# Performance work log

Measured on AMD Instinct MI355X. Metric: run time of the kernel, lower is better.

Reference implementation:

```python
import jax, jax.numpy as jnp
import numpy as np

N, E, B = 50000, 400000, 16
H, D = 4, 64  # heads, per-head out feats
NUM_LAYERS = 4
NEG_SLOPE = 0.2


def setup_inputs() -> dict:
    key = jax.random.key(0)
    ks = jax.random.split(key, 12)
    inp = {
        "feat": jax.random.normal(ks[0], (N, 16), jnp.float32),
        "is_root": jax.random.uniform(ks[1], (N,), jnp.float32),
        "src": jax.random.randint(ks[2], (E,), 0, N, jnp.int32),
        "dst": jax.random.randint(ks[3], (E,), 0, N, jnp.int32),
        "graph_id": jnp.sort(jax.random.randint(ks[4], (N,), 0, B, jnp.int32)),
        "W_in": jax.random.normal(ks[5], (16, 64), jnp.float32) / jnp.sqrt(16.0),
        "b_in": jnp.zeros((64,), jnp.float32),
        "W_src": jax.random.normal(ks[6], (128, 256), jnp.float32) / jnp.sqrt(128.0),
        "b_src": jnp.zeros((256,), jnp.float32),
        "W_dst": jax.random.normal(ks[7], (128, 256), jnp.float32) / jnp.sqrt(128.0),
        "b_dst": jnp.zeros((256,), jnp.float32),
        "attn": jax.random.normal(ks[8], (H, D), jnp.float32) / jnp.sqrt(float(D)),
        "W_out": jax.random.normal(ks[9], (64, 32), jnp.float32) / jnp.sqrt(64.0),
        "b_out": jnp.zeros((32,), jnp.float32),
    }
    return inp


def _gatv2_layer(x, W_src, b_src, W_dst, b_dst, attn, src, dst, n_nodes):
    # DGL GATv2Conv: e_ij = a . LeakyReLU(W_src x_j + W_dst x_i); softmax over in-edges of i.
    fs = (x @ W_src + b_src).reshape(n_nodes, H, D)
    fd = (x @ W_dst + b_dst).reshape(n_nodes, H, D)
    e = jax.nn.leaky_relu(fs[src] + fd[dst], NEG_SLOPE)          # [E,H,D]
    logits = jnp.einsum("ehd,hd->eh", e, attn)                    # [E,H]
    m = jax.ops.segment_max(logits, dst, num_segments=n_nodes)    # [N,H]
    ex = jnp.exp(logits - m[dst])
    denom = jax.ops.segment_sum(ex, dst, num_segments=n_nodes)    # [N,H]
    alpha = ex / denom[dst]                                       # [E,H]
    msg = fs[src] * alpha[:, :, None]                             # [E,H,D]
    rst = jax.ops.segment_sum(msg, dst, num_segments=n_nodes)     # [N,H,D]
    return jnp.tanh(rst)


def reference(feat, is_root, src, dst, graph_id,
              W_in, b_in, W_src, b_src, W_dst, b_dst, attn, W_out, b_out):
    n_nodes = feat.shape[0]
    h0 = feat @ W_in + b_in                                       # [N,64]
    h = h0
    for _ in range(NUM_LAYERS):
        x = jnp.concatenate([h, h0], axis=1)                      # [N,128]
        h = _gatv2_layer(x, W_src, b_src, W_dst, b_dst, attn, src, dst, n_nodes).sum(axis=1)  # [N,64]
    hg = jax.ops.segment_sum(h * is_root[:, None], graph_id, num_segments=B)  # [B,64]
    return hg @ W_out + b_out                                     # [B,32]
```

## Files before the change

### kernel.cpp

```cpp
#include <hip/hip_runtime.h>
#include <math.h>

#define N_NODES 50000
#define N_EDGES 400000
#define N_GRAPHS 16
#define HEADS 4
#define NEG_SLOPE 0.2f
#define MAX_DEG 64

typedef __attribute__((ext_vector_type(8))) short short8;
typedef __attribute__((ext_vector_type(4))) float floatx4;
typedef _Float16 half_t;
typedef _Float16 half2_t __attribute__((ext_vector_type(2)));
typedef _Float16 half4_t __attribute__((ext_vector_type(4)));

__device__ __forceinline__ unsigned short f2bf(float x) {
    union { float f; unsigned int u; } v; v.f = x;
    unsigned int r = v.u + 0x7fffu + ((v.u >> 16) & 1u);
    return (unsigned short)(r >> 16);
}
__device__ __forceinline__ float bf2f(unsigned short b) {
    union { unsigned int u; float f; } v; v.u = ((unsigned int)b) << 16;
    return v.f;
}
__device__ __forceinline__ half2_t u2h2(unsigned int u) {
    union { unsigned int i; half2_t h; } v; v.i = u;
    return v.h;
}
__device__ __forceinline__ float fast_tanh(float x) {
    float e = __expf(2.f * x);
    return 1.f - 2.f / (e + 1.f);
}
__device__ __forceinline__ half2_t lrelu2(half2_t e) {
    half2_t s = e * (half2_t){(half_t)NEG_SLOPE, (half_t)NEG_SLOPE};
    return __builtin_elementwise_max(e, s);
}
__device__ __forceinline__ float dot2acc(half2_t a, half2_t b, float c) {
#if __has_builtin(__builtin_amdgcn_fdot2)
    return __builtin_amdgcn_fdot2(a, b, c, false);
#else
    return c + (float)a[0] * (float)b[0] + (float)a[1] * (float)b[1];
#endif
}

__global__ __launch_bounds__(256) void k_h0_pack(const float* __restrict__ feat,
                                                 const float* __restrict__ W_in,
                                                 const float* __restrict__ b_in,
                                                 unsigned short* __restrict__ h0,
                                                 const float* __restrict__ Wsrc,
                                                 const float* __restrict__ Wdst,
                                                 unsigned short* __restrict__ Wpack,
                                                 int* __restrict__ cursor,
                                                 float* __restrict__ hg) {
    int bid = blockIdx.x;
    if (bid < 12500) {
        int idx = bid * 256 + threadIdx.x;
        int node = idx >> 6, d = idx & 63;
        float acc = b_in[d];
        #pragma unroll
        for (int k = 0; k < 16; k++) acc += feat[node * 16 + k] * W_in[k * 64 + d];
        h0[idx] = f2bf(acc);
    } else if (bid < 12756) {
        int pb = bid - 12500;
        int mat = pb >> 7;
        int idx = (pb & 127) * 256 + threadIdx.x;
        const float* W = mat ? Wdst : Wsrc;
        int j = idx & 7;
        int lane = (idx >> 3) & 63;
        int q = (idx >> 9) & 3;
        int t = (idx >> 11) & 15;
        int col = t * 16 + (lane & 15);
        int k = q * 32 + (lane >> 4) * 8 + j;
        Wpack[mat * 32768 + idx] = f2bf(W[k * 256 + col]);
    } else if (bid < 12952) {
        int idx = (bid - 12756) * 256 + threadIdx.x;
        if (idx < N_NODES) cursor[idx] = 0;
    } else {
        for (int i = threadIdx.x; i < N_GRAPHS * 64; i += 256) hg[i] = 0.f;
    }
}

__global__ __launch_bounds__(256) void k_fill(const int* __restrict__ src, const int* __restrict__ dst,
                                              int* __restrict__ cursor, int* __restrict__ csr_pad, int e) {
    int i = blockIdx.x * 256 + threadIdx.x;
    if (i >= e) return;
    int d = dst[i];
    int slot = atomicAdd(&cursor[d], 1);
    if (slot < MAX_DEG) csr_pad[d * MAX_DEG + slot] = src[i];
}

__global__ __launch_bounds__(256) void k_gemm(const unsigned short* __restrict__ h,
                                              const unsigned short* __restrict__ h0,
                                              const unsigned short* __restrict__ Wpack,
                                              const float* __restrict__ bsrc,
                                              const float* __restrict__ bdst,
                                              half_t* __restrict__ fs,
                                              half_t* __restrict__ fd, int n) {
    __shared__ half_t tile[32][264];
    int mat = blockIdx.y;
    const unsigned short* Wp = Wpack + mat * 32768;
    const float* bias = mat ? bdst : bsrc;
    half_t* out = mat ? fd : fs;
    int wave = threadIdx.x >> 6, lane = threadIdx.x & 63;
    int quad = lane >> 4, m16 = lane & 15;
    int fhalf = wave & 1;
    int ngrp = wave >> 1;
    int node0 = blockIdx.x * 32 + ngrp * 16;

    floatx4 acc[8];
    #pragma unroll
    for (int t = 0; t < 8; t++) acc[t] = (floatx4){0.f, 0.f, 0.f, 0.f};

    int r = node0 + m16;
    if (r > n - 1) r = n - 1;

    #pragma unroll
    for (int q = 0; q < 4; q++) {
        int kk = q * 32 + quad * 8;
        const unsigned short* base = (kk < 64) ? (h + (size_t)r * 64 + kk)
                                               : (h0 + (size_t)r * 64 + (kk - 64));
        short8 x = *(const short8*)base;
        #pragma unroll
        for (int t = 0; t < 8; t++) {
            int tt = fhalf * 8 + t;
            short8 w = *(const short8*)(Wp + ((size_t)(tt * 4 + q) * 64 + lane) * 8);
            acc[t] = __builtin_amdgcn_mfma_f32_16x16x32_bf16(w, x, acc[t], 0, 0, 0);
        }
    }
    int lrow = ngrp * 16 + m16;
    #pragma unroll
    for (int t = 0; t < 8; t++) {
        int fbase = (fhalf * 8 + t) * 16 + quad * 4;
        float4 bb = *(const float4*)(bias + fbase);
        half4_t ov = { (half_t)(acc[t][0] + bb.x), (half_t)(acc[t][1] + bb.y),
                       (half_t)(acc[t][2] + bb.z), (half_t)(acc[t][3] + bb.w) };
        *(half4_t*)&tile[lrow][fbase] = ov;
    }
    __syncthreads();
    int base = blockIdx.x * 32;
    for (int i = threadIdx.x; i < 1024; i += 256) {
        int row = i >> 5, seg = i & 31;
        int node = base + row;
        if (node < n) {
            uint4 v = *(const uint4*)&tile[row][seg * 8];
            *(uint4*)(out + (size_t)node * 256 + seg * 8) = v;
        }
    }
}

__global__ __launch_bounds__(256) void k_agg(const half_t* __restrict__ fs,
                                             const half_t* __restrict__ fd,
                                             const int* __restrict__ cnt,
                                             const int* __restrict__ csr_pad,
                                             const float* __restrict__ attn,
                                             unsigned short* __restrict__ hout, int n) {
    int wave = threadIdx.x >> 6;
    int lane = threadIdx.x & 63;
    int node = blockIdx.x * 4 + wave;
    if (node >= n) return;
    int slot = lane >> 5;
    int foff = ((lane >> 3) & 3) * 64 + (lane & 7) * 8;
    unsigned boff = (unsigned)foff * 2;
    const char* fsb = (const char*)fs;

    int eraw = csr_pad[node * MAX_DEG + lane];
    int deg  = cnt[node];
    uint4 ufd = *(const uint4*)(fd + (size_t)node * 256 + foff);

    half2_t at2[4];
    {
        float4 a0 = *(const float4*)(attn + foff);
        float4 a1 = *(const float4*)(attn + foff + 4);
        at2[0] = (half2_t){(half_t)a0.x, (half_t)a0.y};
        at2[1] = (half2_t){(half_t)a0.z, (half_t)a0.w};
        at2[2] = (half2_t){(half_t)a1.x, (half_t)a1.y};
        at2[3] = (half2_t){(half_t)a1.z, (half_t)a1.w};
    }
    half2_t fd2[4] = {u2h2(ufd.x), u2h2(ufd.y), u2h2(ufd.z), u2h2(ufd.w)};

    if (deg > MAX_DEG) deg = MAX_DEG;
    int eid = (lane < deg) ? eraw : 0;

    float l = 0.f;
    half2_t zero2 = {(half_t)0.f, (half_t)0.f};
    half2_t acc2[4] = {zero2, zero2, zero2, zero2};

    int j = 0;
    do {
        int i0 = j + slot, i1 = j + 2 + slot, i2 = j + 4 + slot, i3 = j + 6 + slot;
        bool v0 = i0 < deg, v1 = i1 < deg, v2 = i2 < deg, v3 = i3 < deg;
        int s0 = __shfl(eid, i0 & 63, 64);
        int s1 = __shfl(eid, i1 & 63, 64);
        int s2 = __shfl(eid, i2 & 63, 64);
        int s3 = __shfl(eid, i3 & 63, 64);
        uint4 g0 = *(const uint4*)(fsb + (((unsigned)s0 << 9) + boff));
        uint4 g1 = *(const uint4*)(fsb + (((unsigned)s1 << 9) + boff));
        uint4 g2 = *(const uint4*)(fsb + (((unsigned)s2 << 9) + boff));
        uint4 g3 = *(const uint4*)(fsb + (((unsigned)s3 << 9) + boff));
        half2_t f0[4] = {u2h2(g0.x), u2h2(g0.y), u2h2(g0.z), u2h2(g0.w)};
        half2_t f1[4] = {u2h2(g1.x), u2h2(g1.y), u2h2(g1.z), u2h2(g1.w)};
        half2_t f2[4] = {u2h2(g2.x), u2h2(g2.y), u2h2(g2.z), u2h2(g2.w)};
        half2_t f3[4] = {u2h2(g3.x), u2h2(g3.y), u2h2(g3.z), u2h2(g3.w)};
        float p0 = 0.f, p1 = 0.f, p2 = 0.f, p3 = 0.f;
        #pragma unroll
        for (int k = 0; k < 4; k++) {
            p0 = dot2acc(at2[k], lrelu2(f0[k] + fd2[k]), p0);
            p1 = dot2acc(at2[k], lrelu2(f1[k] + fd2[k]), p1);
            p2 = dot2acc(at2[k], lrelu2(f2[k] + fd2[k]), p2);
            p3 = dot2acc(at2[k], lrelu2(f3[k] + fd2[k]), p3);
        }
        p0 += __shfl_xor(p0, 1, 64); p1 += __shfl_xor(p1, 1, 64);
        p2 += __shfl_xor(p2, 1, 64); p3 += __shfl_xor(p3, 1, 64);
        p0 += __shfl_xor(p0, 2, 64); p1 += __shfl_xor(p1, 2, 64);
        p2 += __shfl_xor(p2, 2, 64); p3 += __shfl_xor(p3, 2, 64);
        p0 += __shfl_xor(p0, 4, 64); p1 += __shfl_xor(p1, 4, 64);
        p2 += __shfl_xor(p2, 4, 64); p3 += __shfl_xor(p3, 4, 64);
        float w0 = v0 ? __expf(fminf(p0, 80.f)) : 0.f;
        float w1 = v1 ? __expf(fminf(p1, 80.f)) : 0.f;
        float w2 = v2 ? __expf(fminf(p2, 80.f)) : 0.f;
        float w3 = v3 ? __expf(fminf(p3, 80.f)) : 0.f;
        l += (w0 + w1) + (w2 + w3);
        half_t hw0 = (half_t)w0, hw1 = (half_t)w1, hw2 = (half_t)w2, hw3 = (half_t)w3;
        half2_t w02 = {hw0, hw0}, w12 = {hw1, hw1}, w22 = {hw2, hw2}, w32 = {hw3, hw3};
        #pragma unroll
        for (int k = 0; k < 4; k++) {
            acc2[k] += w02 * f0[k];
            acc2[k] += w12 * f1[k];
            acc2[k] += w22 * f2[k];
            acc2[k] += w32 * f3[k];
        }
        j += 8;
    } while (j < deg);
    l += __shfl_xor(l, 32, 64);
    #pragma unroll
    for (int k = 0; k < 4; k++) {
        float t = __builtin_bit_cast(float, acc2[k]);
        t = __shfl_xor(t, 32, 64);
        acc2[k] += __builtin_bit_cast(half2_t, t);
    }

    float inv = (l > 0.f) ? 1.f / l : 0.f;
    half2_t a0 = slot ? acc2[2] : acc2[0];
    half2_t a1 = slot ? acc2[3] : acc2[1];
    float o0 = fast_tanh((float)a0[0] * inv);
    float o1 = fast_tanh((float)a0[1] * inv);
    float o2 = fast_tanh((float)a1[0] * inv);
    float o3 = fast_tanh((float)a1[1] * inv);
    o0 += __shfl_xor(o0, 8, 64);  o0 += __shfl_xor(o0, 16, 64);
    o1 += __shfl_xor(o1, 8, 64);  o1 += __shfl_xor(o1, 16, 64);
    o2 += __shfl_xor(o2, 8, 64);  o2 += __shfl_xor(o2, 16, 64);
    o3 += __shfl_xor(o3, 8, 64);  o3 += __shfl_xor(o3, 16, 64);
    if ((lane & 31) < 8) {
        ushort4 ov = {f2bf(o0), f2bf(o1), f2bf(o2), f2bf(o3)};
        *(ushort4*)(hout + (size_t)node * 64 + (lane & 7) * 8 + slot * 4) = ov;
    }
}

__global__ __launch_bounds__(256) void k_readout(const unsigned short* __restrict__ h,
                                                 const float* __restrict__ is_root,
                                                 const int* __restrict__ gid, float* __restrict__ hg, int n) {
    int wave = threadIdx.x >> 6, lane = threadIdx.x & 63;
    int start = blockIdx.x * 128 + wave * 32;
    if (start >= n) return;
    int stop = min(start + 32, n);
    float acc = 0.f;
    int cur = gid[start];
    for (int i = start; i < stop; i++) {
        int g = gid[i];
        if (g != cur) {
            atomicAdd(&hg[cur * 64 + lane], acc);
            acc = 0.f;
            cur = g;
        }
        acc += bf2f(h[(size_t)i * 64 + lane]) * is_root[i];
    }
    atomicAdd(&hg[cur * 64 + lane], acc);
}

__global__ __launch_bounds__(512) void k_out(const float* __restrict__ hg, const float* __restrict__ W_out,
                                             const float* __restrict__ b_out, float* __restrict__ out) {
    int t = threadIdx.x;
    if (t >= N_GRAPHS * 32) return;
    int b = t >> 5, c = t & 31;
    float a = b_out[c];
    #pragma unroll
    for (int d = 0; d < 64; d++) a += hg[b * 64 + d] * W_out[d * 32 + c];
    out[t] = a;
}

extern "C" void kernel_launch(void* const* d_in, const int* in_sizes, int n_in,
                              void* d_out, int out_size, void* d_ws, size_t ws_size,
                              hipStream_t stream) {
    const float* feat    = (const float*)d_in[0];
    const float* is_root = (const float*)d_in[1];
    const int*   src     = (const int*)d_in[2];
    const int*   dst     = (const int*)d_in[3];
    const int*   gid     = (const int*)d_in[4];
    const float* W_in    = (const float*)d_in[5];
    const float* b_in    = (const float*)d_in[6];
    const float* W_src   = (const float*)d_in[7];
    const float* b_src   = (const float*)d_in[8];
    const float* W_dst   = (const float*)d_in[9];
    const float* b_dst   = (const float*)d_in[10];
    const float* attn    = (const float*)d_in[11];
    const float* W_out   = (const float*)d_in[12];
    const float* b_out   = (const float*)d_in[13];
    float* out = (float*)d_out;

    char* ws = (char*)d_ws;
    size_t off = 0;
    auto take = [&](size_t bytes) -> char* {
        char* p = ws + off;
        off = (off + bytes + 255) & ~(size_t)255;
        return p;
    };
    half_t* fs            = (half_t*)take((size_t)N_NODES * 256 * 2);
    half_t* fd            = (half_t*)take((size_t)N_NODES * 256 * 2);
    unsigned short* h0    = (unsigned short*)take((size_t)N_NODES * 64 * 2);
    unsigned short* hA    = (unsigned short*)take((size_t)N_NODES * 64 * 2);
    unsigned short* hB    = (unsigned short*)take((size_t)N_NODES * 64 * 2);
    unsigned short* Wpack = (unsigned short*)take((size_t)2 * 32768 * 2);
    float* hg             = (float*)take((size_t)N_GRAPHS * 64 * 4);
    int*   cursor         = (int*)take((size_t)N_NODES * 4);
    int*   csr_pad        = (int*)take((size_t)N_NODES * MAX_DEG * 4);

    const int n = N_NODES, e = N_EDGES;
    dim3 b256(256);

    k_h0_pack<<<dim3(12953), b256, 0, stream>>>(feat, W_in, b_in, h0, W_src, W_dst, Wpack, cursor, hg);

    k_fill<<<dim3((e + 255) / 256), b256, 0, stream>>>(src, dst, cursor, csr_pad, e);

    const unsigned short* hin = h0;
    unsigned short* houts[4] = { hA, hB, hA, hB };
    for (int layer = 0; layer < 4; layer++) {
        k_gemm<<<dim3((n + 31) / 32, 2), b256, 0, stream>>>(hin, h0, Wpack, b_src, b_dst, fs, fd, n);
        k_agg<<<dim3((n + 3) / 4), b256, 0, stream>>>(fs, fd, cursor, csr_pad, attn, houts[layer], n);
        hin = houts[layer];
    }

    k_readout<<<dim3((n + 127) / 128), b256, 0, stream>>>(hB, is_root, gid, hg, n);
    k_out<<<dim3(1), dim3(512), 0, stream>>>(hg, W_out, b_out, out);
}
```

Before: 377.5 us.

## Fuse GAT aggregation with next layer's projection GEMM and readout

The separate aggregation and GEMM kernels are merged into one per-layer kernel. Each block of 32 nodes aggregates neighbours into a shared-memory h tile, then runs the MFMA projection for the next layer directly from that tile, which removes the round trip of h through global memory. The final layer's aggregation is fused with the graph readout, and fs/fd are double-buffered because the fused kernel reads one set while writing the other. In exchange, each wave now handles 8 nodes serially with one-ahead prefetch, which lowers parallelism, and more shared memory per block may reduce occupancy.

```diff
diff --git a/kernel.cpp b/kernel.cpp
--- a/kernel.cpp
+++ b/kernel.cpp
@@ -7,6 +7,7 @@
 #define HEADS 4
 #define NEG_SLOPE 0.2f
 #define MAX_DEG 64
+#define NTILES 1563
 
 typedef __attribute__((ext_vector_type(8))) short short8;
 typedef __attribute__((ext_vector_type(4))) float floatx4;
@@ -41,6 +42,79 @@
 #else
     return c + (float)a[0] * (float)b[0] + (float)a[1] * (float)b[1];
 #endif
+}
+
+__device__ __forceinline__ void agg_node(const char* __restrict__ fsb,
+                                         const half2_t* at2, const half2_t* fd2,
+                                         int eid, int deg, int slot, unsigned boff,
+                                         float* o) {
+    float l = 0.f;
+    half2_t zero2 = {(half_t)0.f, (half_t)0.f};
+    half2_t acc2[4] = {zero2, zero2, zero2, zero2};
+    int j = 0;
+    do {
+        int i0 = j + slot, i1 = j + 2 + slot, i2 = j + 4 + slot, i3 = j + 6 + slot;
+        bool v0 = i0 < deg, v1 = i1 < deg, v2 = i2 < deg, v3 = i3 < deg;
+        int s0 = __shfl(eid, i0 & 63, 64);
+        int s1 = __shfl(eid, i1 & 63, 64);
+        int s2 = __shfl(eid, i2 & 63, 64);
+        int s3 = __shfl(eid, i3 & 63, 64);
+        uint4 g0 = *(const uint4*)(fsb + (((unsigned)s0 << 9) + boff));
+        uint4 g1 = *(const uint4*)(fsb + (((unsigned)s1 << 9) + boff));
+        uint4 g2 = *(const uint4*)(fsb + (((unsigned)s2 << 9) + boff));
+        uint4 g3 = *(const uint4*)(fsb + (((unsigned)s3 << 9) + boff));
+        half2_t f0[4] = {u2h2(g0.x), u2h2(g0.y), u2h2(g0.z), u2h2(g0.w)};
+        half2_t f1[4] = {u2h2(g1.x), u2h2(g1.y), u2h2(g1.z), u2h2(g1.w)};
+        half2_t f2[4] = {u2h2(g2.x), u2h2(g2.y), u2h2(g2.z), u2h2(g2.w)};
+        half2_t f3[4] = {u2h2(g3.x), u2h2(g3.y), u2h2(g3.z), u2h2(g3.w)};
+        float p0 = 0.f, p1 = 0.f, p2 = 0.f, p3 = 0.f;
+        #pragma unroll
+        for (int k = 0; k < 4; k++) {
+            p0 = dot2acc(at2[k], lrelu2(f0[k] + fd2[k]), p0);
+            p1 = dot2acc(at2[k], lrelu2(f1[k] + fd2[k]), p1);
+            p2 = dot2acc(at2[k], lrelu2(f2[k] + fd2[k]), p2);
+            p3 = dot2acc(at2[k], lrelu2(f3[k] + fd2[k]), p3);
+        }
+        p0 += __shfl_xor(p0, 1, 64); p1 += __shfl_xor(p1, 1, 64);
+        p2 += __shfl_xor(p2, 1, 64); p3 += __shfl_xor(p3, 1, 64);
+        p0 += __shfl_xor(p0, 2, 64); p1 += __shfl_xor(p1, 2, 64);
+        p2 += __shfl_xor(p2, 2, 64); p3 += __shfl_xor(p3, 2, 64);
+        p0 += __shfl_xor(p0, 4, 64); p1 += __shfl_xor(p1, 4, 64);
+        p2 += __shfl_xor(p2, 4, 64); p3 += __shfl_xor(p3, 4, 64);
+        float w0 = v0 ? __expf(fminf(p0, 80.f)) : 0.f;
+        float w1 = v1 ? __expf(fminf(p1, 80.f)) : 0.f;
+        float w2 = v2 ? __expf(fminf(p2, 80.f)) : 0.f;
+        float w3 = v3 ? __expf(fminf(p3, 80.f)) : 0.f;
+        l += (w0 + w1) + (w2 + w3);
+        half_t hw0 = (half_t)w0, hw1 = (half_t)w1, hw2 = (half_t)w2, hw3 = (half_t)w3;
+        half2_t w02 = {hw0, hw0}, w12 = {hw1, hw1}, w22 = {hw2, hw2}, w32 = {hw3, hw3};
+        #pragma unroll
+        for (int k = 0; k < 4; k++) {
+            acc2[k] += w02 * f0[k];
+            acc2[k] += w12 * f1[k];
+            acc2[k] += w22 * f2[k];
+            acc2[k] += w32 * f3[k];
+        }
+        j += 8;
+    } while (j < deg);
+    l += __shfl_xor(l, 32, 64);
+    #pragma unroll
+    for (int k = 0; k < 4; k++) {
+        float t = __builtin_bit_cast(float, acc2[k]);
+        t = __shfl_xor(t, 32, 64);
+        acc2[k] += __builtin_bit_cast(half2_t, t);
+    }
+    float inv = (l > 0.f) ? 1.f / l : 0.f;
+    half2_t a0 = slot ? acc2[2] : acc2[0];
+    half2_t a1 = slot ? acc2[3] : acc2[1];
+    o[0] = fast_tanh((float)a0[0] * inv);
+    o[1] = fast_tanh((float)a0[1] * inv);
+    o[2] = fast_tanh((float)a1[0] * inv);
+    o[3] = fast_tanh((float)a1[1] * inv);
+    o[0] += __shfl_xor(o[0], 8, 64);  o[0] += __shfl_xor(o[0], 16, 64);
+    o[1] += __shfl_xor(o[1], 8, 64);  o[1] += __shfl_xor(o[1], 16, 64);
+    o[2] += __shfl_xor(o[2], 8, 64);  o[2] += __shfl_xor(o[2], 16, 64);
+    o[3] += __shfl_xor(o[3], 8, 64);  o[3] += __shfl_xor(o[3], 16, 64);
 }
 
 __global__ __launch_bounds__(256) void k_h0_pack(const float* __restrict__ feat,
@@ -148,133 +222,183 @@
     }
 }
 
-__global__ __launch_bounds__(256) void k_agg(const half_t* __restrict__ fs,
-                                             const half_t* __restrict__ fd,
-                                             const int* __restrict__ cnt,
-                                             const int* __restrict__ csr_pad,
-                                             const float* __restrict__ attn,
-                                             unsigned short* __restrict__ hout, int n) {
-    int wave = threadIdx.x >> 6;
-    int lane = threadIdx.x & 63;
-    int node = blockIdx.x * 4 + wave;
-    if (node >= n) return;
-    int slot = lane >> 5;
-    int foff = ((lane >> 3) & 3) * 64 + (lane & 7) * 8;
-    unsigned boff = (unsigned)foff * 2;
-    const char* fsb = (const char*)fs;
-
-    int eraw = csr_pad[node * MAX_DEG + lane];
-    int deg  = cnt[node];
-    uint4 ufd = *(const uint4*)(fd + (size_t)node * 256 + foff);
-
-    half2_t at2[4];
+__global__ __launch_bounds__(256) void k_layer(
+    const half_t* __restrict__ fs_in, const half_t* __restrict__ fd_in,
+    const int* __restrict__ cnt, const int* __restrict__ csr_pad,
+    const float* __restrict__ attn,
+    const unsigned short* __restrict__ h0,
+    const unsigned short* __restrict__ Wpack,
+    const float* __restrict__ bsrc, const float* __restrict__ bdst,
+    half_t* __restrict__ fs_out, half_t* __restrict__ fd_out, int n)
+{
+    __shared__ half_t tile[32][264];
+    __shared__ unsigned short h_tile[32][72];
+    const int tid = threadIdx.x;
+    const int wave = tid >> 6, lane = tid & 63;
+    const int tile_base = blockIdx.x * 32;
+
     {
-        float4 a0 = *(const float4*)(attn + foff);
-        float4 a1 = *(const float4*)(attn + foff + 4);
-        at2[0] = (half2_t){(half_t)a0.x, (half_t)a0.y};
-        at2[1] = (half2_t){(half_t)a0.z, (half_t)a0.w};
-        at2[2] = (half2_t){(half_t)a1.x, (half_t)a1.y};
-        at2[3] = (half2_t){(half_t)a1.z, (half_t)a1.w};
-    }
-    half2_t fd2[4] = {u2h2(ufd.x), u2h2(ufd.y), u2h2(ufd.z), u2h2(ufd.w)};
-
-    if (deg > MAX_DEG) deg = MAX_DEG;
-    int eid = (lane < deg) ? eraw : 0;
-
-    float l = 0.f;
-    half2_t zero2 = {(half_t)0.f, (half_t)0.f};
-    half2_t acc2[4] = {zero2, zero2, zero2, zero2};
-
-    int j = 0;
-    do {
-        int i0 = j + slot, i1 = j + 2 + slot, i2 = j + 4 + slot, i3 = j + 6 + slot;
-        bool v0 = i0 < deg, v1 = i1 < deg, v2 = i2 < deg, v3 = i3 < deg;
-        int s0 = __shfl(eid, i0 & 63, 64);
-        int s1 = __shfl(eid, i1 & 63, 64);
-        int s2 = __shfl(eid, i2 & 63, 64);
-        int s3 = __shfl(eid, i3 & 63, 64);
-        uint4 g0 = *(const uint4*)(fsb + (((unsigned)s0 << 9) + boff));
-        uint4 g1 = *(const uint4*)(fsb + (((unsigned)s1 << 9) + boff));
-        uint4 g2 = *(const uint4*)(fsb + (((unsigned)s2 << 9) + boff));
-        uint4 g3 = *(const uint4*)(fsb + (((unsigned)s3 << 9) + boff));
-        half2_t f0[4] = {u2h2(g0.x), u2h2(g0.y), u2h2(g0.z), u2h2(g0.w)};
-        half2_t f1[4] = {u2h2(g1.x), u2h2(g1.y), u2h2(g1.z), u2h2(g1.w)};
-        half2_t f2[4] = {u2h2(g2.x), u2h2(g2.y), u2h2(g2.z), u2h2(g2.w)};
-        half2_t f3[4] = {u2h2(g3.x), u2h2(g3.y), u2h2(g3.z), u2h2(g3.w)};
-        float p0 = 0.f, p1 = 0.f, p2 = 0.f, p3 = 0.f;
-        #pragma unroll
-        for (int k = 0; k < 4; k++) {
-            p0 = dot2acc(at2[k], lrelu2(f0[k] + fd2[k]), p0);
-            p1 = dot2acc(at2[k], lrelu2(f1[k] + fd2[k]), p1);
-            p2 = dot2acc(at2[k], lrelu2(f2[k] + fd2[k]), p2);
-            p3 = dot2acc(at2[k], lrelu2(f3[k] + fd2[k]), p3);
-        }
-        p0 += __shfl_xor(p0, 1, 64); p1 += __shfl_xor(p1, 1, 64);
-        p2 += __shfl_xor(p2, 1, 64); p3 += __shfl_xor(p3, 1, 64);
-        p0 += __shfl_xor(p0, 2, 64); p1 += __shfl_xor(p1, 2, 64);
-        p2 += __shfl_xor(p2, 2, 64); p3 += __shfl_xor(p3, 2, 64);
-        p0 += __shfl_xor(p0, 4, 64); p1 += __shfl_xor(p1, 4, 64);
-        p2 += __shfl_xor(p2, 4, 64); p3 += __shfl_xor(p3, 4, 64);
-        float w0 = v0 ? __expf(fminf(p0, 80.f)) : 0.f;
-        float w1 = v1 ? __expf(fminf(p1, 80.f)) : 0.f;
-        float w2 = v2 ? __expf(fminf(p2, 80.f)) : 0.f;
-        float w3 = v3 ? __expf(fminf(p3, 80.f)) : 0.f;
-        l += (w0 + w1) + (w2 + w3);
-        half_t hw0 = (half_t)w0, hw1 = (half_t)w1, hw2 = (half_t)w2, hw3 = (half_t)w3;
-        half2_t w02 = {hw0, hw0}, w12 = {hw1, hw1}, w22 = {hw2, hw2}, w32 = {hw3, hw3};
-        #pragma unroll
-        for (int k = 0; k < 4; k++) {
-            acc2[k] += w02 * f0[k];
-            acc2[k] += w12 * f1[k];
-            acc2[k] += w22 * f2[k];
-            acc2[k] += w32 * f3[k];
-        }
-        j += 8;
-    } while (j < deg);
-    l += __shfl_xor(l, 32, 64);
-    #pragma unroll
-    for (int k = 0; k < 4; k++) {
-        float t = __builtin_bit_cast(float, acc2[k]);
-        t = __shfl_xor(t, 32, 64);
-        acc2[k] += __builtin_bit_cast(half2_t, t);
-    }
-
-    float inv = (l > 0.f) ? 1.f / l : 0.f;
-    half2_t a0 = slot ? acc2[2] : acc2[0];
-    half2_t a1 = slot ? acc2[3] : acc2[1];
-    float o0 = fast_tanh((float)a0[0] * inv);
-    float o1 = fast_tanh((float)a0[1] * inv);
-    float o2 = fast_tanh((float)a1[0] * inv);
-    float o3 = fast_tanh((float)a1[1] * inv);
-    o0 += __shfl_xor(o0, 8, 64);  o0 += __shfl_xor(o0, 16, 64);
-    o1 += __shfl_xor(o1, 8, 64);  o1 += __shfl_xor(o1, 16, 64);
-    o2 += __shfl_xor(o2, 8, 64);  o2 += __shfl_xor(o2, 16, 64);
-    o3 += __shfl_xor(o3, 8, 64);  o3 += __shfl_xor(o3, 16, 64);
-    if ((lane & 31) < 8) {
-        ushort4 ov = {f2bf(o0), f2bf(o1), f2bf(o2), f2bf(o3)};
-        *(ushort4*)(hout + (size_t)node * 64 + (lane & 7) * 8 + slot * 4) = ov;
-    }
-}
-
-__global__ __launch_bounds__(256) void k_readout(const unsigned short* __restrict__ h,
-                                                 const float* __restrict__ is_root,
-                                                 const int* __restrict__ gid, float* __restrict__ hg, int n) {
-    int wave = threadIdx.x >> 6, lane = threadIdx.x & 63;
-    int start = blockIdx.x * 128 + wave * 32;
-    if (start >= n) return;
-    int stop = min(start + 32, n);
-    float acc = 0.f;
-    int cur = gid[start];
-    for (int i = start; i < stop; i++) {
-        int g = gid[i];
-        if (g != cur) {
-            atomicAdd(&hg[cur * 64 + lane], acc);
-            acc = 0.f;
-            cur = g;
-        }
-        acc += bf2f(h[(size_t)i * 64 + lane]) * is_root[i];
-    }
-    atomicAdd(&hg[cur * 64 + lane], acc);
+        const int slot = lane >> 5;
+        const int foff = ((lane >> 3) & 3) * 64 + (lane & 7) * 8;
+        const unsigned boff = (unsigned)foff * 2;
+        const char* fsb = (const char*)fs_in;
+        half2_t at2[4];
+        {
+            float4 a0 = *(const float4*)(attn + foff);
+            float4 a1 = *(const float4*)(attn + foff + 4);
+            at2[0] = (half2_t){(half_t)a0.x, (half_t)a0.y};
+            at2[1] = (half2_t){(half_t)a0.z, (half_t)a0.w};
+            at2[2] = (half2_t){(half_t)a1.x, (half_t)a1.y};
+            at2[3] = (half2_t){(half_t)a1.z, (half_t)a1.w};
+        }
+        int gbase = tile_base + wave * 8;
+        int pn = gbase; if (pn > n - 1) pn = n - 1;
+        int eraw = csr_pad[pn * MAX_DEG + lane];
+        int degn = cnt[pn];
+        uint4 ufd = *(const uint4*)(fd_in + (size_t)pn * 256 + foff);
+        for (int nd = 0; nd < 8; nd++) {
+            int ceraw = eraw, cdeg = degn;
+            uint4 cufd = ufd;
+            if (nd < 7) {
+                int nx = gbase + nd + 1; if (nx > n - 1) nx = n - 1;
+                eraw = csr_pad[nx * MAX_DEG + lane];
+                degn = cnt[nx];
+                ufd = *(const uint4*)(fd_in + (size_t)nx * 256 + foff);
+            }
+            half2_t fd2[4] = {u2h2(cufd.x), u2h2(cufd.y), u2h2(cufd.z), u2h2(cufd.w)};
+            if (cdeg > MAX_DEG) cdeg = MAX_DEG;
+            int eid = (lane < cdeg) ? ceraw : 0;
+            float o[4];
+            agg_node(fsb, at2, fd2, eid, cdeg, slot, boff, o);
+            if ((lane & 31) < 8) {
+                ushort4 ov = {f2bf(o[0]), f2bf(o[1]), f2bf(o[2]), f2bf(o[3])};
+                *(ushort4*)&h_tile[wave * 8 + nd][(lane & 7) * 8 + slot * 4] = ov;
+            }
+        }
+    }
+    __syncthreads();
+
+    const int quad = lane >> 4, m16 = lane & 15;
+    const int fhalf = wave & 1, ngrp = wave >> 1;
+    int lrow = ngrp * 16 + m16;
+    int r = tile_base + lrow;
+    if (r > n - 1) r = n - 1;
+
+    short8 x[4];
+    x[0] = *(const short8*)&h_tile[lrow][quad * 8];
+    x[1] = *(const short8*)&h_tile[lrow][32 + quad * 8];
+    x[2] = *(const short8*)(h0 + (size_t)r * 64 + quad * 8);
+    x[3] = *(const short8*)(h0 + (size_t)r * 64 + 32 + quad * 8);
+
+    #pragma unroll
+    for (int mat = 0; mat < 2; mat++) {
+        const unsigned short* Wp = Wpack + mat * 32768;
+        const float* bias = mat ? bdst : bsrc;
+        half_t* outp = mat ? fd_out : fs_out;
+
+        floatx4 acc[8];
+        #pragma unroll
+        for (int t = 0; t < 8; t++) acc[t] = (floatx4){0.f, 0.f, 0.f, 0.f};
+
+        #pragma unroll
+        for (int q = 0; q < 4; q++) {
+            #pragma unroll
+            for (int t = 0; t < 8; t++) {
+                int tt = fhalf * 8 + t;
+                short8 wv = *(const short8*)(Wp + ((size_t)(tt * 4 + q) * 64 + lane) * 8);
+                acc[t] = __builtin_amdgcn_mfma_f32_16x16x32_bf16(wv, x[q], acc[t], 0, 0, 0);
+            }
+        }
+        #pragma unroll
+        for (int t = 0; t < 8; t++) {
+            int fbase = (fhalf * 8 + t) * 16 + quad * 4;
+            float4 bb = *(const float4*)(bias + fbase);
+            half4_t ov = { (half_t)(acc[t][0] + bb.x), (half_t)(acc[t][1] + bb.y),
+                           (half_t)(acc[t][2] + bb.z), (half_t)(acc[t][3] + bb.w) };
+            *(half4_t*)&tile[lrow][fbase] = ov;
+        }
+        __syncthreads();
+        for (int i = tid; i < 1024; i += 256) {
+            int row = i >> 5, seg = i & 31;
+            int node = tile_base + row;
+            if (node < n) {
+                uint4 v = *(const uint4*)&tile[row][seg * 8];
+                *(uint4*)(outp + (size_t)node * 256 + seg * 8) = v;
+            }
+        }
+        if (mat == 0) __syncthreads();
+    }
+}
+
+__global__ __launch_bounds__(256) void k_aggro(
+    const half_t* __restrict__ fs_in, const half_t* __restrict__ fd_in,
+    const int* __restrict__ cnt, const int* __restrict__ csr_pad,
+    const float* __restrict__ attn,
+    const float* __restrict__ is_root, const int* __restrict__ gid,
+    float* __restrict__ hg, int n)
+{
+    __shared__ unsigned short h_tile[32][72];
+    const int tid = threadIdx.x;
+    const int wave = tid >> 6, lane = tid & 63;
+    const int tile_base = blockIdx.x * 32;
+
+    {
+        const int slot = lane >> 5;
+        const int foff = ((lane >> 3) & 3) * 64 + (lane & 7) * 8;
+        const unsigned boff = (unsigned)foff * 2;
+        const char* fsb = (const char*)fs_in;
+        half2_t at2[4];
+        {
+            float4 a0 = *(const float4*)(attn + foff);
+            float4 a1 = *(const float4*)(attn + foff + 4);
+            at2[0] = (half2_t){(half_t)a0.x, (half_t)a0.y};
+            at2[1] = (half2_t){(half_t)a0.z, (half_t)a0.w};
+            at2[2] = (half2_t){(half_t)a1.x, (half_t)a1.y};
+            at2[3] = (half2_t){(half_t)a1.z, (half_t)a1.w};
+        }
+        int gbase = tile_base + wave * 8;
+        int pn = gbase; if (pn > n - 1) pn = n - 1;
+        int eraw = csr_pad[pn * MAX_DEG + lane];
+        int degn = cnt[pn];
+        uint4 ufd = *(const uint4*)(fd_in + (size_t)pn * 256 + foff);
+        for (int nd = 0; nd < 8; nd++) {
+            int ceraw = eraw, cdeg = degn;
+            uint4 cufd = ufd;
+            if (nd < 7) {
+                int nx = gbase + nd + 1; if (nx > n - 1) nx = n - 1;
+                eraw = csr_pad[nx * MAX_DEG + lane];
+                degn = cnt[nx];
+                ufd = *(const uint4*)(fd_in + (size_t)nx * 256 + foff);
+            }
+            half2_t fd2[4] = {u2h2(cufd.x), u2h2(cufd.y), u2h2(cufd.z), u2h2(cufd.w)};
+            if (cdeg > MAX_DEG) cdeg = MAX_DEG;
+            int eid = (lane < cdeg) ? ceraw : 0;
+            float o[4];
+            agg_node(fsb, at2, fd2, eid, cdeg, slot, boff, o);
+            if ((lane & 31) < 8) {
+                ushort4 ov = {f2bf(o[0]), f2bf(o[1]), f2bf(o[2]), f2bf(o[3])};
+                *(ushort4*)&h_tile[wave * 8 + nd][(lane & 7) * 8 + slot * 4] = ov;
+            }
+        }
+    }
+    __syncthreads();
+
+    int gbase = tile_base + wave * 8;
+    if (gbase < n) {
+        int stop = gbase + 8; if (stop > n) stop = n;
+        float racc = 0.f;
+        int cur = gid[gbase];
+        for (int i = gbase; i < stop; i++) {
+            int g = gid[i];
+            if (g != cur) {
+                atomicAdd(&hg[cur * 64 + lane], racc);
+                racc = 0.f;
+                cur = g;
+            }
+            racc += bf2f(h_tile[i - tile_base][lane]) * is_root[i];
+        }
+        atomicAdd(&hg[cur * 64 + lane], racc);
+    }
 }
 
 __global__ __launch_bounds__(512) void k_out(const float* __restrict__ hg, const float* __restrict__ W_out,
@@ -314,11 +438,11 @@
         off = (off + bytes + 255) & ~(size_t)255;
         return p;
     };
-    half_t* fs            = (half_t*)take((size_t)N_NODES * 256 * 2);
-    half_t* fd            = (half_t*)take((size_t)N_NODES * 256 * 2);
+    half_t* fsA           = (half_t*)take((size_t)N_NODES * 256 * 2);
+    half_t* fdA           = (half_t*)take((size_t)N_NODES * 256 * 2);
+    half_t* fsB           = (half_t*)take((size_t)N_NODES * 256 * 2);
+    half_t* fdB           = (half_t*)take((size_t)N_NODES * 256 * 2);
     unsigned short* h0    = (unsigned short*)take((size_t)N_NODES * 64 * 2);
-    unsigned short* hA    = (unsigned short*)take((size_t)N_NODES * 64 * 2);
-    unsigned short* hB    = (unsigned short*)take((size_t)N_NODES * 64 * 2);
     unsigned short* Wpack = (unsigned short*)take((size_t)2 * 32768 * 2);
     float* hg             = (float*)take((size_t)N_GRAPHS * 64 * 4);
     int*   cursor         = (int*)take((size_t)N_NODES * 4);
@@ -328,17 +452,16 @@
     dim3 b256(256);
 
     k_h0_pack<<<dim3(12953), b256, 0, stream>>>(feat, W_in, b_in, h0, W_src, W_dst, Wpack, cursor, hg);
-
     k_fill<<<dim3((e + 255) / 256), b256, 0, stream>>>(src, dst, cursor, csr_pad, e);
 
-    const unsigned short* hin = h0;
-    unsigned short* houts[4] = { hA, hB, hA, hB };
-    for (int layer = 0; layer < 4; layer++) {
-        k_gemm<<<dim3((n + 31) / 32, 2), b256, 0, stream>>>(hin, h0, Wpack, b_src, b_dst, fs, fd, n);
-        k_agg<<<dim3((n + 3) / 4), b256, 0, stream>>>(fs, fd, cursor, csr_pad, attn, houts[layer], n);
-        hin = houts[layer];
-    }
-
-    k_readout<<<dim3((n + 127) / 128), b256, 0, stream>>>(hB, is_root, gid, hg, n);
+    k_gemm<<<dim3(NTILES, 2), b256, 0, stream>>>(h0, h0, Wpack, b_src, b_dst, fsA, fdA, n);
+    k_layer<<<dim3(NTILES), b256, 0, stream>>>(fsA, fdA, cursor, csr_pad, attn, h0, Wpack,
+                                               b_src, b_dst, fsB, fdB, n);
+    k_layer<<<dim3(NTILES), b256, 0, stream>>>(fsB, fdB, cursor, csr_pad, attn, h0, Wpack,
+                                               b_src, b_dst, fsA, fdA, n);
+    k_layer<<<dim3(NTILES), b256, 0, stream>>>(fsA, fdA, cursor, csr_pad, attn, h0, Wpack,
+                                               b_src, b_dst, fsB, fdB, n);
+    k_aggro<<<dim3(NTILES), b256, 0, stream>>>(fsB, fdB, cursor, csr_pad, attn, is_root, gid, hg, n);
+
     k_out<<<dim3(1), dim3(512), 0, stream>>>(hg, W_out, b_out, out);
 }
```

Result: slower. 418.7 us (+10.9%).
